# Performance work log

Measured on AMD Instinct MI355X. Metric: run time of the kernel, lower is better.

The kernel has to match this reference:

```python
import jax, jax.numpy as jnp
import numpy as np

N, E, DIM, HEADS = 40000, 640000, 128, 8
HD = DIM // HEADS  # per-head dim
NEG_SLOPE = 0.2


def setup_inputs() -> dict:
    key = jax.random.key(0)
    ks = jax.random.split(key, 10)
    s = 1.0 / np.sqrt(DIM)
    return {
        "x": jax.random.normal(ks[0], (N, DIM), dtype=jnp.float32),
        "edge_index": jax.random.randint(ks[1], (2, E), 0, N, dtype=jnp.int64),
        "W_src": jax.random.normal(ks[2], (DIM, DIM), dtype=jnp.float32) * s,
        "b_src": jnp.zeros((DIM,), dtype=jnp.float32),
        "W_dst": jax.random.normal(ks[3], (DIM, DIM), dtype=jnp.float32) * s,
        "b_dst": jnp.zeros((DIM,), dtype=jnp.float32),
        "att": jax.random.normal(ks[4], (HEADS, HD), dtype=jnp.float32) * (1.0 / np.sqrt(HD)),
        "bias_out": jnp.zeros((DIM,), dtype=jnp.float32),
        "ln_gamma": jnp.ones((DIM,), dtype=jnp.float32),
        "ln_beta": jnp.zeros((DIM,), dtype=jnp.float32),
    }


def reference(x, edge_index, W_src, b_src, W_dst, b_dst, att, bias_out, ln_gamma, ln_beta):
    n = x.shape[0]
    # PyG GATv2Conv default: add self loops
    loops = jnp.arange(n, dtype=edge_index.dtype)
    src = jnp.concatenate([edge_index[0], loops])  # message source j
    dst = jnp.concatenate([edge_index[1], loops])  # message target i

    xs = (x @ W_src + b_src).reshape(n, HEADS, HD)  # [N,H,C]
    xd = (x @ W_dst + b_dst).reshape(n, HEADS, HD)

    # per-edge GATv2 attention logits
    e = xs[src] + xd[dst]                                   # [Et,H,C]
    e = jnp.where(e >= 0, e, NEG_SLOPE * e)                 # LeakyReLU(0.2)
    logits = jnp.einsum('ehc,hc->eh', e, att)               # [Et,H]

    # segment softmax over incoming edges of each dst node
    m = jax.ops.segment_max(logits, dst, num_segments=n)    # [N,H]
    ex = jnp.exp(logits - m[dst])
    denom = jax.ops.segment_sum(ex, dst, num_segments=n)    # [N,H]
    alpha = ex / denom[dst]                                  # [Et,H]

    # weighted scatter-add of source features
    msg = xs[src] * alpha[:, :, None]                       # [Et,H,C]
    out = jax.ops.segment_sum(msg, dst, num_segments=n)     # [N,H,C]
    out = out.reshape(n, DIM) + bias_out

    # dropout is identity in eval mode; residual + LayerNorm + GELU
    h = out + x
    mu = jnp.mean(h, axis=-1, keepdims=True)
    var = jnp.var(h, axis=-1, keepdims=True)
    h = (h - mu) / jnp.sqrt(var + 1e-5) * ln_gamma + ln_beta
    return jax.nn.gelu(h, approximate=False)
```

## Files before the change

kernel.cpp:

```cpp
#include <hip/hip_runtime.h>

typedef unsigned int uint;
typedef unsigned short ushort;
typedef __attribute__((ext_vector_type(8))) short short8;
typedef __attribute__((ext_vector_type(4))) float f32x4;
typedef __attribute__((ext_vector_type(2))) float f32x2;

__device__ __forceinline__ float b2f(ushort u) {
    return __uint_as_float(((uint)u) << 16);
}
__device__ __forceinline__ ushort f2b(float f) {
    uint u = __float_as_uint(f);
    u += 0x7FFFu + ((u >> 16) & 1u);
    return (ushort)(u >> 16);
}
__device__ __forceinline__ float fast_exp2(float v) {
    float r;
    asm volatile("v_exp_f32 %0, %1" : "=v"(r) : "v"(v));
    return r;
}
__device__ __forceinline__ f32x2 unpk(uint u) {
    f32x2 o;
    o.x = __uint_as_float(u << 16);
    o.y = __uint_as_float(u & 0xFFFF0000u);
    return o;
}
__device__ __forceinline__ f32x2 pmax0(f32x2 a) {
#if __has_builtin(__builtin_elementwise_max)
    return __builtin_elementwise_max(a, (f32x2)(0.f));
#else
    f32x2 o; o.x = fmaxf(a.x, 0.f); o.y = fmaxf(a.y, 0.f); return o;
#endif
}
__device__ __forceinline__ f32x2 pmin0(f32x2 a) {
#if __has_builtin(__builtin_elementwise_min)
    return __builtin_elementwise_min(a, (f32x2)(0.f));
#else
    f32x2 o; o.x = fminf(a.x, 0.f); o.y = fminf(a.y, 0.f); return o;
#endif
}

template<int CTRL>
__device__ __forceinline__ float dpp_add(float v) {
    int s = __float_as_int(v);
    int d = __builtin_amdgcn_update_dpp(s, s, CTRL, 0xF, 0xF, true);
    return v + __int_as_float(d);
}

#define LDW 136

__global__ __launch_bounds__(256) void gemm_kernel(
    const float* __restrict__ x,
    const float* __restrict__ Wsrc, const float* __restrict__ bsrc,
    const float* __restrict__ Wdst, const float* __restrict__ bdst,
    ushort* __restrict__ xs, float* __restrict__ xd,
    int n, int* __restrict__ deg)
{
    __shared__ ushort WtS[128 * LDW];
    __shared__ ushort WtD[128 * LDW];
    int t = threadIdx.x;
    int gid = blockIdx.x * 256 + t;
    if (gid < n) deg[gid] = 1;
    for (int i = t; i < 128 * 128; i += 256) {
        int k = i >> 7, c = i & 127;
        WtS[c * LDW + k] = f2b(Wsrc[i]);
        WtD[c * LDW + k] = f2b(Wdst[i]);
    }
    __syncthreads();

    int wave = t >> 6, lane = t & 63;
    int r = lane & 15, q = lane >> 4;
    int row = blockIdx.x * 64 + wave * 16 + r;
    f32x4 accS[8], accD[8];
#pragma unroll
    for (int i = 0; i < 8; i++) { accS[i] = (f32x4)(0.f); accD[i] = (f32x4)(0.f); }

#pragma unroll
    for (int kk = 0; kk < 4; kk++) {
        float v[8];
#pragma unroll
        for (int j = 0; j < 8; j++) v[j] = 0.f;
        if (row < n) {
            const float4* src = (const float4*)(x + (long)row * 128 + kk * 32 + q * 8);
            float4 p0 = src[0], p1 = src[1];
            v[0] = p0.x; v[1] = p0.y; v[2] = p0.z; v[3] = p0.w;
            v[4] = p1.x; v[5] = p1.y; v[6] = p1.z; v[7] = p1.w;
        }
        short8 ah, al;
#pragma unroll
        for (int j = 0; j < 8; j++) {
            ushort h = f2b(v[j]);
            ah[j] = (short)h;
            al[j] = (short)f2b(v[j] - b2f(h));
        }
#pragma unroll
        for (int ct = 0; ct < 8; ct++) {
            int off = (ct * 16 + r) * LDW + kk * 32 + q * 8;
            short8 bS = *(const short8*)(WtS + off);
            short8 bD = *(const short8*)(WtD + off);
            accS[ct] = __builtin_amdgcn_mfma_f32_16x16x32_bf16(ah, bS, accS[ct], 0, 0, 0);
            accS[ct] = __builtin_amdgcn_mfma_f32_16x16x32_bf16(al, bS, accS[ct], 0, 0, 0);
            accD[ct] = __builtin_amdgcn_mfma_f32_16x16x32_bf16(ah, bD, accD[ct], 0, 0, 0);
            accD[ct] = __builtin_amdgcn_mfma_f32_16x16x32_bf16(al, bD, accD[ct], 0, 0, 0);
        }
    }
    int rbase = blockIdx.x * 64 + wave * 16 + q * 4;
#pragma unroll
    for (int ct = 0; ct < 8; ct++) {
        int col = ct * 16 + r;
        float bS = bsrc[col];
        float bD = bdst[col];
#pragma unroll
        for (int rg = 0; rg < 4; rg++) {
            int orow = rbase + rg;
            if (orow < n) {
                xs[(long)orow * 128 + col] = f2b(accS[ct][rg] + bS);
                xd[(long)orow * 128 + col] = accD[ct][rg] + bD;
            }
        }
    }
}

__global__ void count_kernel(const int* __restrict__ ei, int E,
                             int* __restrict__ deg) {
    __shared__ int f_s;
    if (threadIdx.x < 64) {
        int w = ei[2 * threadIdx.x + 1];
        unsigned long long nz = __ballot(w != 0);
        if (threadIdx.x == 0) f_s = (nz == 0ULL) ? 1 : 0;
    }
    __syncthreads();
    int f = f_s;
    int e = blockIdx.x * 256 + threadIdx.x;
    if (e < E) {
        int d = f ? ei[2 * E + 2 * e] : ei[E + e];
        atomicAdd(&deg[d], 1);
    }
}

__global__ __launch_bounds__(1024) void scan_blk(
    const int* __restrict__ deg, int* __restrict__ lpre,
    int* __restrict__ bsum, int n)
{
    __shared__ int ws[16];
    __shared__ int wp[16];
    int t = threadIdx.x, lane = t & 63, w = t >> 6;
    int g = blockIdx.x * 1024 + t;
    int v = (g < n) ? deg[g] : 0;
    int inc = v;
#pragma unroll
    for (int off = 1; off < 64; off <<= 1) {
        int sh = __shfl_up(inc, off);
        if (lane >= off) inc += sh;
    }
    if (lane == 63) ws[w] = inc;
    __syncthreads();
    if (t == 0) {
        int run = 0;
#pragma unroll
        for (int i = 0; i < 16; i++) { wp[i] = run; run += ws[i]; }
        bsum[blockIdx.x] = run;
    }
    __syncthreads();
    if (g < n) lpre[g] = wp[w] + inc - v;
}

__global__ __launch_bounds__(1024) void scan_fix(
    const int* __restrict__ lpre, const int* __restrict__ bsum,
    const int* __restrict__ deg, int* __restrict__ row_start,
    int* __restrict__ cursor, int n)
{
    __shared__ int boff_s;
    int t = threadIdx.x, b = blockIdx.x;
    if (t < 64) {
        int v = 0;
        for (int i = t; i < b; i += 64) v += bsum[i];
#pragma unroll
        for (int off = 32; off >= 1; off >>= 1) v += __shfl_xor(v, off);
        if (t == 0) boff_s = v;
    }
    __syncthreads();
    int g = b * 1024 + t;
    if (g < n) {
        int rs = lpre[g] + boff_s;
        row_start[g] = rs;
        cursor[g] = rs;
        if (g == n - 1) row_start[n] = rs + deg[g];
    }
}

__global__ void fill_kernel(const int* __restrict__ ei, int E, int n,
                            int* __restrict__ cursor, int* __restrict__ esrc) {
    __shared__ int f_s;
    if (threadIdx.x < 64) {
        int w = ei[2 * threadIdx.x + 1];
        unsigned long long nz = __ballot(w != 0);
        if (threadIdx.x == 0) f_s = (nz == 0ULL) ? 1 : 0;
    }
    __syncthreads();
    int f = f_s;
    int idx = blockIdx.x * 256 + threadIdx.x;
    if (idx < E) {
        int s = f ? ei[2 * idx]         : ei[idx];
        int d = f ? ei[2 * E + 2 * idx] : ei[E + idx];
        int pos = atomicAdd(&cursor[d], 1);
        esrc[pos] = s;
    } else if (idx < E + n) {
        int i = idx - E;
        int pos = atomicAdd(&cursor[i], 1);
        esrc[pos] = i;
    }
}

__global__ __launch_bounds__(256) void node_kernel(
    const ushort* __restrict__ xs, const float* __restrict__ xd,
    const float* __restrict__ x,  const float* __restrict__ att,
    const float* __restrict__ bias_out, const float* __restrict__ gamma,
    const float* __restrict__ beta,
    const int* __restrict__ row_start, const int* __restrict__ esrc,
    float* __restrict__ out, int n)
{
    int lane = threadIdx.x & 63;
    int node = blockIdx.x * 4 + (threadIdx.x >> 6);
    if (node >= n) return;
    int q = lane >> 4, r = lane & 15;
    int cb = r * 8;

    const float LOG2E = 1.44269504088896f;
    f32x2 xd8[4], at8[4];
    {
        const float4* xp = (const float4*)(xd + (long)node * 128 + cb);
        float4 p0 = xp[0], p1 = xp[1];
        xd8[0].x = p0.x; xd8[0].y = p0.y; xd8[1].x = p0.z; xd8[1].y = p0.w;
        xd8[2].x = p1.x; xd8[2].y = p1.y; xd8[3].x = p1.z; xd8[3].y = p1.w;
        const float4* ap = (const float4*)(att + cb);
        float4 a0 = ap[0], a1 = ap[1];
        at8[0].x = a0.x * LOG2E; at8[0].y = a0.y * LOG2E;
        at8[1].x = a0.z * LOG2E; at8[1].y = a0.w * LOG2E;
        at8[2].x = a1.x * LOG2E; at8[2].y = a1.y * LOG2E;
        at8[3].x = a1.z * LOG2E; at8[3].y = a1.w * LOG2E;
    }

    int start = row_start[node], end = row_start[node + 1];
    int end1 = end - 1;
    f32x2 a8[4];
#pragma unroll
    for (int i = 0; i < 4; i++) a8[i] = (f32x2)(0.f);
    float s = 0.f;

    int j0 = esrc[min(start + q, end1)];
    uint4 raw = *(const uint4*)(xs + (long)j0 * 128 + cb);

    for (int base = start; base < end; base += 4) {
        int jn = esrc[min(base + 4 + q, end1)];
        uint4 rawn = *(const uint4*)(xs + (long)jn * 128 + cb);

        f32x2 v0 = unpk(raw.x), v1 = unpk(raw.y), v2 = unpk(raw.z), v3 = unpk(raw.w);
        f32x2 t0 = v0 + xd8[0], t1 = v1 + xd8[1], t2 = v2 + xd8[2], t3 = v3 + xd8[3];
        t0 = pmax0(t0) + 0.2f * pmin0(t0);
        t1 = pmax0(t1) + 0.2f * pmin0(t1);
        t2 = pmax0(t2) + 0.2f * pmin0(t2);
        t3 = pmax0(t3) + 0.2f * pmin0(t3);
        f32x2 d2 = t0 * at8[0];
        d2 += t1 * at8[1];
        d2 += t2 * at8[2];
        d2 += t3 * at8[3];
        float d = d2.x + d2.y;
        d = dpp_add<0xB1>(d);
        float p = fast_exp2(d);
        p = (base + q < end) ? p : 0.f;
        s += p;
        a8[0] += p * v0; a8[1] += p * v1; a8[2] += p * v2; a8[3] += p * v3;

        raw = rawn;
    }

#pragma unroll
    for (int off = 16; off <= 32; off <<= 1) {
        s += __shfl_xor(s, off);
#pragma unroll
        for (int i = 0; i < 4; i++) {
            a8[i].x += __shfl_xor(a8[i].x, off);
            a8[i].y += __shfl_xor(a8[i].y, off);
        }
    }

    float inv = 1.f / s;
    f32x2 o8[4];
    {
        const float4* bp = (const float4*)(bias_out + cb);
        const float4* xp = (const float4*)(x + (long)node * 128 + cb);
        float4 b0 = bp[0], b1 = bp[1], x0 = xp[0], x1 = xp[1];
        o8[0].x = a8[0].x * inv + b0.x + x0.x; o8[0].y = a8[0].y * inv + b0.y + x0.y;
        o8[1].x = a8[1].x * inv + b0.z + x0.z; o8[1].y = a8[1].y * inv + b0.w + x0.w;
        o8[2].x = a8[2].x * inv + b1.x + x1.x; o8[2].y = a8[2].y * inv + b1.y + x1.y;
        o8[3].x = a8[3].x * inv + b1.z + x1.z; o8[3].y = a8[3].y * inv + b1.w + x1.w;
    }
    float ssum = 0.f, ssq = 0.f;
#pragma unroll
    for (int i = 0; i < 4; i++) {
        ssum += o8[i].x + o8[i].y;
        ssq  += o8[i].x * o8[i].x + o8[i].y * o8[i].y;
    }
#pragma unroll
    for (int off = 1; off <= 8; off <<= 1) {
        ssum += __shfl_xor(ssum, off);
        ssq  += __shfl_xor(ssq, off);
    }
    float mean = ssum * (1.f / 128.f);
    float var  = ssq  * (1.f / 128.f) - mean * mean;
    float rstd = rsqrtf(var + 1e-5f);

    if (q == 0) {
        const float4* gp = (const float4*)(gamma + cb);
        const float4* ep = (const float4*)(beta + cb);
        float4 g0 = gp[0], g1 = gp[1], e0 = ep[0], e1 = ep[1];
        float gch[8] = {g0.x, g0.y, g0.z, g0.w, g1.x, g1.y, g1.z, g1.w};
        float ech[8] = {e0.x, e0.y, e0.z, e0.w, e1.x, e1.y, e1.z, e1.w};
        float och[8] = {o8[0].x, o8[0].y, o8[1].x, o8[1].y,
                        o8[2].x, o8[2].y, o8[3].x, o8[3].y};
        float res[8];
#pragma unroll
        for (int i = 0; i < 8; i++) {
            float g = (och[i] - mean) * rstd * gch[i] + ech[i];
            res[i] = 0.5f * g * (1.f + erff(g * 0.70710678118654752f));
        }
        float4* op = (float4*)(out + (long)node * 128 + cb);
        float4 r0, r1;
        r0.x = res[0]; r0.y = res[1]; r0.z = res[2]; r0.w = res[3];
        r1.x = res[4]; r1.y = res[5]; r1.z = res[6]; r1.w = res[7];
        op[0] = r0; op[1] = r1;
    }
}

extern "C" void kernel_launch(void* const* d_in, const int* in_sizes, int n_in,
                              void* d_out, int out_size, void* d_ws, size_t ws_size,
                              hipStream_t stream)
{
    const float* x    = (const float*)d_in[0];
    const int*   ei   = (const int*)d_in[1];
    const float* Wsrc = (const float*)d_in[2];
    const float* bsrc = (const float*)d_in[3];
    const float* Wdst = (const float*)d_in[4];
    const float* bdst = (const float*)d_in[5];
    const float* att  = (const float*)d_in[6];
    const float* bout = (const float*)d_in[7];
    const float* gam  = (const float*)d_in[8];
    const float* bet  = (const float*)d_in[9];
    float* out = (float*)d_out;

    int n = in_sizes[0] / 128;
    int E = in_sizes[1] / 2;

    char* p = (char*)d_ws;
    auto alloc = [&](size_t bytes) {
        char* q = p;
        p += (bytes + 255) & ~((size_t)255);
        return q;
    };
    ushort* xs        = (ushort*)alloc((size_t)n * 128 * 2);
    float*  xd        = (float*)alloc((size_t)n * 128 * 4);
    int*    deg       = (int*)alloc((size_t)n * 4);
    int*    row_start = (int*)alloc((size_t)(n + 1) * 4);
    int*    cursor    = (int*)alloc((size_t)n * 4);
    int*    esrc      = (int*)alloc((size_t)(E + n) * 4);
    int     nblk      = (n + 1023) / 1024;
    int*    lpre      = (int*)alloc((size_t)nblk * 1024 * 4);
    int*    bsum      = (int*)alloc((size_t)nblk * 4);

    hipLaunchKernelGGL(gemm_kernel, dim3((n + 63) / 64), dim3(256), 0, stream,
                       x, Wsrc, bsrc, Wdst, bdst, xs, xd, n, deg);
    hipLaunchKernelGGL(count_kernel, dim3((E + 255) / 256), dim3(256), 0, stream,
                       ei, E, deg);
    hipLaunchKernelGGL(scan_blk, dim3(nblk), dim3(1024), 0, stream,
                       deg, lpre, bsum, n);
    hipLaunchKernelGGL(scan_fix, dim3(nblk), dim3(1024), 0, stream,
                       lpre, bsum, deg, row_start, cursor, n);
    hipLaunchKernelGGL(fill_kernel, dim3((E + n + 255) / 256), dim3(256), 0, stream,
                       ei, E, n, cursor, esrc);
    hipLaunchKernelGGL(node_kernel, dim3((n + 3) / 4), dim3(256), 0, stream,
                       xs, xd, x, att, bout, gam, bet, row_start, esrc, out, n);
}
```

Baseline: 231.4 us.

## Rewrite GATv2 logit via abs identity, retile GEMM, single-wave node blocks

The per-edge LeakyReLU dot product is rewritten as 0.6*x + 0.4*|x|. The att·xd term is hoisted out of the edge loop as a per-node constant, which removes the max/min ops in the inner loop. The GEMM kernel now uses 512-thread blocks of 128 rows and loads weights as float4 during transposition. The node kernel launches one 64-thread block per node and uses 32-bit index arithmetic for gathers. The block reshaping changes occupancy and scheduling, and the algebraic rewrite slightly changes rounding.

```diff
diff --git a/kernel.cpp b/kernel.cpp
--- a/kernel.cpp
+++ b/kernel.cpp
@@ -4,7 +4,6 @@
 typedef unsigned short ushort;
 typedef __attribute__((ext_vector_type(8))) short short8;
 typedef __attribute__((ext_vector_type(4))) float f32x4;
-typedef __attribute__((ext_vector_type(2))) float f32x2;
 
 __device__ __forceinline__ float b2f(ushort u) {
     return __uint_as_float(((uint)u) << 16);
@@ -18,26 +17,6 @@
     float r;
     asm volatile("v_exp_f32 %0, %1" : "=v"(r) : "v"(v));
     return r;
-}
-__device__ __forceinline__ f32x2 unpk(uint u) {
-    f32x2 o;
-    o.x = __uint_as_float(u << 16);
-    o.y = __uint_as_float(u & 0xFFFF0000u);
-    return o;
-}
-__device__ __forceinline__ f32x2 pmax0(f32x2 a) {
-#if __has_builtin(__builtin_elementwise_max)
-    return __builtin_elementwise_max(a, (f32x2)(0.f));
-#else
-    f32x2 o; o.x = fmaxf(a.x, 0.f); o.y = fmaxf(a.y, 0.f); return o;
-#endif
-}
-__device__ __forceinline__ f32x2 pmin0(f32x2 a) {
-#if __has_builtin(__builtin_elementwise_min)
-    return __builtin_elementwise_min(a, (f32x2)(0.f));
-#else
-    f32x2 o; o.x = fminf(a.x, 0.f); o.y = fminf(a.y, 0.f); return o;
-#endif
 }
 
 template<int CTRL>
@@ -49,7 +28,7 @@
 
 #define LDW 136
 
-__global__ __launch_bounds__(256) void gemm_kernel(
+__global__ __launch_bounds__(512) void gemm_kernel(
     const float* __restrict__ x,
     const float* __restrict__ Wsrc, const float* __restrict__ bsrc,
     const float* __restrict__ Wdst, const float* __restrict__ bdst,
@@ -59,18 +38,26 @@
     __shared__ ushort WtS[128 * LDW];
     __shared__ ushort WtD[128 * LDW];
     int t = threadIdx.x;
-    int gid = blockIdx.x * 256 + t;
+    int gid = blockIdx.x * 512 + t;
     if (gid < n) deg[gid] = 1;
-    for (int i = t; i < 128 * 128; i += 256) {
+    for (int i = t * 4; i < 128 * 128; i += 512 * 4) {
         int k = i >> 7, c = i & 127;
-        WtS[c * LDW + k] = f2b(Wsrc[i]);
-        WtD[c * LDW + k] = f2b(Wdst[i]);
+        float4 wS = *(const float4*)(Wsrc + i);
+        float4 wD = *(const float4*)(Wdst + i);
+        WtS[(c + 0) * LDW + k] = f2b(wS.x);
+        WtS[(c + 1) * LDW + k] = f2b(wS.y);
+        WtS[(c + 2) * LDW + k] = f2b(wS.z);
+        WtS[(c + 3) * LDW + k] = f2b(wS.w);
+        WtD[(c + 0) * LDW + k] = f2b(wD.x);
+        WtD[(c + 1) * LDW + k] = f2b(wD.y);
+        WtD[(c + 2) * LDW + k] = f2b(wD.z);
+        WtD[(c + 3) * LDW + k] = f2b(wD.w);
     }
     __syncthreads();
 
     int wave = t >> 6, lane = t & 63;
     int r = lane & 15, q = lane >> 4;
-    int row = blockIdx.x * 64 + wave * 16 + r;
+    int row = blockIdx.x * 128 + wave * 16 + r;
     f32x4 accS[8], accD[8];
 #pragma unroll
     for (int i = 0; i < 8; i++) { accS[i] = (f32x4)(0.f); accD[i] = (f32x4)(0.f); }
@@ -81,7 +68,7 @@
 #pragma unroll
         for (int j = 0; j < 8; j++) v[j] = 0.f;
         if (row < n) {
-            const float4* src = (const float4*)(x + (long)row * 128 + kk * 32 + q * 8);
+            const float4* src = (const float4*)(x + (size_t)row * 128 + kk * 32 + q * 8);
             float4 p0 = src[0], p1 = src[1];
             v[0] = p0.x; v[1] = p0.y; v[2] = p0.z; v[3] = p0.w;
             v[4] = p1.x; v[5] = p1.y; v[6] = p1.z; v[7] = p1.w;
@@ -104,7 +91,7 @@
             accD[ct] = __builtin_amdgcn_mfma_f32_16x16x32_bf16(al, bD, accD[ct], 0, 0, 0);
         }
     }
-    int rbase = blockIdx.x * 64 + wave * 16 + q * 4;
+    int rbase = blockIdx.x * 128 + wave * 16 + q * 4;
 #pragma unroll
     for (int ct = 0; ct < 8; ct++) {
         int col = ct * 16 + r;
@@ -114,8 +101,8 @@
         for (int rg = 0; rg < 4; rg++) {
             int orow = rbase + rg;
             if (orow < n) {
-                xs[(long)orow * 128 + col] = f2b(accS[ct][rg] + bS);
-                xd[(long)orow * 128 + col] = accD[ct][rg] + bD;
+                xs[(size_t)orow * 128 + col] = f2b(accS[ct][rg] + bS);
+                xd[(size_t)orow * 128 + col] = accD[ct][rg] + bD;
             }
         }
     }
@@ -212,7 +199,7 @@
     }
 }
 
-__global__ __launch_bounds__(256) void node_kernel(
+__global__ __launch_bounds__(64) void node_kernel(
     const ushort* __restrict__ xs, const float* __restrict__ xd,
     const float* __restrict__ x,  const float* __restrict__ att,
     const float* __restrict__ bias_out, const float* __restrict__ gamma,
@@ -220,57 +207,64 @@
     const int* __restrict__ row_start, const int* __restrict__ esrc,
     float* __restrict__ out, int n)
 {
-    int lane = threadIdx.x & 63;
-    int node = blockIdx.x * 4 + (threadIdx.x >> 6);
+    int lane = threadIdx.x;
+    int node = blockIdx.x;
     if (node >= n) return;
     int q = lane >> 4, r = lane & 15;
     int cb = r * 8;
 
     const float LOG2E = 1.44269504088896f;
-    f32x2 xd8[4], at8[4];
+    const float A = 0.6f * LOG2E, B = 0.4f * LOG2E;
+
+    float xdc[8], atc[8];
     {
-        const float4* xp = (const float4*)(xd + (long)node * 128 + cb);
+        const float4* xp = (const float4*)(xd + (size_t)node * 128 + cb);
         float4 p0 = xp[0], p1 = xp[1];
-        xd8[0].x = p0.x; xd8[0].y = p0.y; xd8[1].x = p0.z; xd8[1].y = p0.w;
-        xd8[2].x = p1.x; xd8[2].y = p1.y; xd8[3].x = p1.z; xd8[3].y = p1.w;
+        xdc[0]=p0.x; xdc[1]=p0.y; xdc[2]=p0.z; xdc[3]=p0.w;
+        xdc[4]=p1.x; xdc[5]=p1.y; xdc[6]=p1.z; xdc[7]=p1.w;
         const float4* ap = (const float4*)(att + cb);
         float4 a0 = ap[0], a1 = ap[1];
-        at8[0].x = a0.x * LOG2E; at8[0].y = a0.y * LOG2E;
-        at8[1].x = a0.z * LOG2E; at8[1].y = a0.w * LOG2E;
-        at8[2].x = a1.x * LOG2E; at8[2].y = a1.y * LOG2E;
-        at8[3].x = a1.z * LOG2E; at8[3].y = a1.w * LOG2E;
-    }
+        atc[0]=a0.x; atc[1]=a0.y; atc[2]=a0.z; atc[3]=a0.w;
+        atc[4]=a1.x; atc[5]=a1.y; atc[6]=a1.z; atc[7]=a1.w;
+    }
+    float KL = 0.f;
+#pragma unroll
+    for (int i = 0; i < 8; i++) KL = fmaf(atc[i], xdc[i], KL);
+    KL *= A;
 
     int start = row_start[node], end = row_start[node + 1];
     int end1 = end - 1;
-    f32x2 a8[4];
-#pragma unroll
-    for (int i = 0; i < 4; i++) a8[i] = (f32x2)(0.f);
-    float s = 0.f;
-
+    float s = 0.f, acc[8];
+#pragma unroll
+    for (int i = 0; i < 8; i++) acc[i] = 0.f;
+
+    uint cboff = (uint)(cb);
     int j0 = esrc[min(start + q, end1)];
-    uint4 raw = *(const uint4*)(xs + (long)j0 * 128 + cb);
+    uint4 raw = *(const uint4*)(xs + (uint)j0 * 128u + cboff);
 
     for (int base = start; base < end; base += 4) {
         int jn = esrc[min(base + 4 + q, end1)];
-        uint4 rawn = *(const uint4*)(xs + (long)jn * 128 + cb);
-
-        f32x2 v0 = unpk(raw.x), v1 = unpk(raw.y), v2 = unpk(raw.z), v3 = unpk(raw.w);
-        f32x2 t0 = v0 + xd8[0], t1 = v1 + xd8[1], t2 = v2 + xd8[2], t3 = v3 + xd8[3];
-        t0 = pmax0(t0) + 0.2f * pmin0(t0);
-        t1 = pmax0(t1) + 0.2f * pmin0(t1);
-        t2 = pmax0(t2) + 0.2f * pmin0(t2);
-        t3 = pmax0(t3) + 0.2f * pmin0(t3);
-        f32x2 d2 = t0 * at8[0];
-        d2 += t1 * at8[1];
-        d2 += t2 * at8[2];
-        d2 += t3 * at8[3];
-        float d = d2.x + d2.y;
-        d = dpp_add<0xB1>(d);
-        float p = fast_exp2(d);
+        uint4 rawn = *(const uint4*)(xs + (uint)jn * 128u + cboff);
+
+        float v[8];
+        v[0] = __uint_as_float(raw.x << 16); v[1] = __uint_as_float(raw.x & 0xFFFF0000u);
+        v[2] = __uint_as_float(raw.y << 16); v[3] = __uint_as_float(raw.y & 0xFFFF0000u);
+        v[4] = __uint_as_float(raw.z << 16); v[5] = __uint_as_float(raw.z & 0xFFFF0000u);
+        v[6] = __uint_as_float(raw.w << 16); v[7] = __uint_as_float(raw.w & 0xFFFF0000u);
+
+        float dv = 0.f, da = 0.f;
+#pragma unroll
+        for (int i = 0; i < 8; i++) {
+            dv = fmaf(atc[i], v[i], dv);
+            da = fmaf(atc[i], fabsf(v[i] + xdc[i]), da);
+        }
+        float P = fmaf(A, dv, fmaf(B, da, KL));
+        P = dpp_add<0xB1>(P);
+        float p = fast_exp2(P);
         p = (base + q < end) ? p : 0.f;
         s += p;
-        a8[0] += p * v0; a8[1] += p * v1; a8[2] += p * v2; a8[3] += p * v3;
+#pragma unroll
+        for (int i = 0; i < 8; i++) acc[i] = fmaf(p, v[i], acc[i]);
 
         raw = rawn;
     }
@@ -279,28 +273,25 @@
     for (int off = 16; off <= 32; off <<= 1) {
         s += __shfl_xor(s, off);
 #pragma unroll
-        for (int i = 0; i < 4; i++) {
-            a8[i].x += __shfl_xor(a8[i].x, off);
-            a8[i].y += __shfl_xor(a8[i].y, off);
-        }
+        for (int i = 0; i < 8; i++) acc[i] += __shfl_xor(acc[i], off);
     }
 
     float inv = 1.f / s;
-    f32x2 o8[4];
+    float o[8];
     {
         const float4* bp = (const float4*)(bias_out + cb);
-        const float4* xp = (const float4*)(x + (long)node * 128 + cb);
+        const float4* xp = (const float4*)(x + (size_t)node * 128 + cb);
         float4 b0 = bp[0], b1 = bp[1], x0 = xp[0], x1 = xp[1];
-        o8[0].x = a8[0].x * inv + b0.x + x0.x; o8[0].y = a8[0].y * inv + b0.y + x0.y;
-        o8[1].x = a8[1].x * inv + b0.z + x0.z; o8[1].y = a8[1].y * inv + b0.w + x0.w;
-        o8[2].x = a8[2].x * inv + b1.x + x1.x; o8[2].y = a8[2].y * inv + b1.y + x1.y;
-        o8[3].x = a8[3].x * inv + b1.z + x1.z; o8[3].y = a8[3].y * inv + b1.w + x1.w;
+        o[0] = fmaf(acc[0], inv, b0.x + x0.x); o[1] = fmaf(acc[1], inv, b0.y + x0.y);
+        o[2] = fmaf(acc[2], inv, b0.z + x0.z); o[3] = fmaf(acc[3], inv, b0.w + x0.w);
+        o[4] = fmaf(acc[4], inv, b1.x + x1.x); o[5] = fmaf(acc[5], inv, b1.y + x1.y);
+        o[6] = fmaf(acc[6], inv, b1.z + x1.z); o[7] = fmaf(acc[7], inv, b1.w + x1.w);
     }
     float ssum = 0.f, ssq = 0.f;
 #pragma unroll
-    for (int i = 0; i < 4; i++) {
-        ssum += o8[i].x + o8[i].y;
-        ssq  += o8[i].x * o8[i].x + o8[i].y * o8[i].y;
+    for (int i = 0; i < 8; i++) {
+        ssum += o[i];
+        ssq  = fmaf(o[i], o[i], ssq);
     }
 #pragma unroll
     for (int off = 1; off <= 8; off <<= 1) {
@@ -317,15 +308,13 @@
         float4 g0 = gp[0], g1 = gp[1], e0 = ep[0], e1 = ep[1];
         float gch[8] = {g0.x, g0.y, g0.z, g0.w, g1.x, g1.y, g1.z, g1.w};
         float ech[8] = {e0.x, e0.y, e0.z, e0.w, e1.x, e1.y, e1.z, e1.w};
-        float och[8] = {o8[0].x, o8[0].y, o8[1].x, o8[1].y,
-                        o8[2].x, o8[2].y, o8[3].x, o8[3].y};
         float res[8];
 #pragma unroll
         for (int i = 0; i < 8; i++) {
-            float g = (och[i] - mean) * rstd * gch[i] + ech[i];
+            float g = (o[i] - mean) * rstd * gch[i] + ech[i];
             res[i] = 0.5f * g * (1.f + erff(g * 0.70710678118654752f));
         }
-        float4* op = (float4*)(out + (long)node * 128 + cb);
+        float4* op = (float4*)(out + (size_t)node * 128 + cb);
         float4 r0, r1;
         r0.x = res[0]; r0.y = res[1]; r0.z = res[2]; r0.w = res[3];
         r1.x = res[4]; r1.y = res[5]; r1.z = res[6]; r1.w = res[7];
@@ -368,7 +357,7 @@
     int*    lpre      = (int*)alloc((size_t)nblk * 1024 * 4);
     int*    bsum      = (int*)alloc((size_t)nblk * 4);
 
-    hipLaunchKernelGGL(gemm_kernel, dim3((n + 63) / 64), dim3(256), 0, stream,
+    hipLaunchKernelGGL(gemm_kernel, dim3((n + 127) / 128), dim3(512), 0, stream,
                        x, Wsrc, bsrc, Wdst, bdst, xs, xd, n, deg);
     hipLaunchKernelGGL(count_kernel, dim3((E + 255) / 256), dim3(256), 0, stream,
                        ei, E, deg);
@@ -378,6 +367,6 @@
                        lpre, bsum, deg, row_start, cursor, n);
     hipLaunchKernelGGL(fill_kernel, dim3((E + n + 255) / 256), dim3(256), 0, stream,
                        ei, E, n, cursor, esrc);
-    hipLaunchKernelGGL(node_kernel, dim3((n + 3) / 4), dim3(256), 0, stream,
+    hipLaunchKernelGGL(node_kernel, dim3(n), dim3(64), 0, stream,
                        xs, xd, x, att, bout, gam, bet, row_start, esrc, out, n);
 }
```

Measured after the change: 221.4 us. -4.3%, faster.
